# Kernel optimization log

Hardware: AMD Instinct MI355X
Metric: run time of the kernel (lower is better)

Reference implementation:

```python
import jax, jax.numpy as jnp
import numpy as np
import math

# model / graph sizes
N_NODES, N_EDGES = 50000, 400000
IN_DIM, N_HID = 256, 128
NUM_TYPES, NUM_REL = 4, 5
N_HEADS, D_K = 4, 32
N_LAYERS, MAX_LEN = 2, 240
SQRT_DK = math.sqrt(D_K)


def _gelu(x):
    return jax.nn.gelu(x, approximate=False)  # torch F.gelu is exact erf


def _per_type_linear(x, types, W, b):
    # x:[n,din], types:[n] int, W:[T,din,dout], b:[T,dout]
    out = jnp.zeros((x.shape[0], W.shape[-1]), x.dtype)
    for t in range(W.shape[0]):  # small fixed type count
        out = jnp.where((types == t)[:, None], x @ W[t] + b[t], out)
    return out


def setup_inputs() -> dict:
    key = jax.random.key(0)
    ks = jax.random.split(key, 16)
    node_feature = jax.random.normal(ks[0], (N_NODES, IN_DIM), jnp.float32)
    node_type = jax.random.randint(ks[1], (N_NODES,), 0, NUM_TYPES)
    edge_index = jax.random.randint(ks[2], (2, N_EDGES), 0, N_NODES)
    edge_type = jax.random.randint(ks[3], (N_EDGES,), 0, NUM_REL)
    edge_time = jax.random.randint(ks[4], (N_EDGES,), 0, MAX_LEN)

    def w(k, shape, s=0.05):
        return jax.random.normal(k, shape, jnp.float32) * s

    adapt_W = w(ks[5], (NUM_TYPES, IN_DIM, N_HID))
    adapt_b = jnp.zeros((NUM_TYPES, N_HID), jnp.float32)
    Wk = w(ks[6], (N_LAYERS, NUM_TYPES, N_HID, N_HID))
    Wq = w(ks[7], (N_LAYERS, NUM_TYPES, N_HID, N_HID))
    Wv = w(ks[8], (N_LAYERS, NUM_TYPES, N_HID, N_HID))
    Wa = w(ks[9], (N_LAYERS, NUM_TYPES, N_HID, N_HID))
    bk = jnp.zeros((N_LAYERS, NUM_TYPES, N_HID), jnp.float32)
    bq = jnp.zeros((N_LAYERS, NUM_TYPES, N_HID), jnp.float32)
    bv = jnp.zeros((N_LAYERS, NUM_TYPES, N_HID), jnp.float32)
    ba = jnp.zeros((N_LAYERS, NUM_TYPES, N_HID), jnp.float32)
    rel_pri = jnp.ones((N_LAYERS, NUM_REL, N_HEADS), jnp.float32)
    rel_att = w(ks[10], (N_LAYERS, NUM_REL, N_HEADS, D_K, D_K), 0.1) + jnp.eye(D_K, dtype=jnp.float32)
    rel_msg = w(ks[11], (N_LAYERS, NUM_REL, N_HEADS, D_K, D_K), 0.1) + jnp.eye(D_K, dtype=jnp.float32)
    skip = jnp.ones((N_LAYERS, NUM_TYPES), jnp.float32)
    # fixed sinusoidal RTE table (pyHGT RelTemporalEncoding, requires_grad=False)
    pos = np.arange(MAX_LEN, dtype=np.float32)[:, None]
    div = np.exp(np.arange(0, N_HID, 2, dtype=np.float32) * -(math.log(10000.0) / N_HID))
    tab = np.zeros((MAX_LEN, N_HID), np.float32)
    tab[:, 0::2] = np.sin(pos * div) / math.sqrt(N_HID)
    tab[:, 1::2] = np.cos(pos * div) / math.sqrt(N_HID)
    rte_emb = jnp.asarray(tab)
    rte_W = w(ks[12], (N_LAYERS, N_HID, N_HID))
    rte_b = jnp.zeros((N_LAYERS, N_HID), jnp.float32)
    return dict(node_feature=node_feature, adapt_W=adapt_W, adapt_b=adapt_b,
                Wk=Wk, bk=bk, Wq=Wq, bq=bq, Wv=Wv, bv=bv, Wa=Wa, ba=ba,
                rel_pri=rel_pri, rel_att=rel_att, rel_msg=rel_msg, skip=skip,
                rte_emb=rte_emb, rte_W=rte_W, rte_b=rte_b,
                node_type=node_type, edge_index=edge_index,
                edge_type=edge_type, edge_time=edge_time)


def reference(node_feature, adapt_W, adapt_b, Wk, bk, Wq, bq, Wv, bv, Wa, ba,
              rel_pri, rel_att, rel_msg, skip, rte_emb, rte_W, rte_b,
              node_type, edge_index, edge_type, edge_time):
    n = node_feature.shape[0]
    src, dst = edge_index[0], edge_index[1]  # PyG: row0 = source j, row1 = target i
    st, tt = node_type[src], node_type[dst]
    # per-type input adaptation (all types use Linear + GELU)
    h = _gelu(_per_type_linear(node_feature, node_type, adapt_W, adapt_b))  # [N, n_hid]
    for l in range(N_LAYERS):  # HGTConv stack
        x_j, x_i = h[src], h[dst]
        s_e = x_j + rte_emb[edge_time] @ rte_W[l] + rte_b[l]  # RTE on source per edge
        k = _per_type_linear(s_e, st, Wk[l], bk[l]).reshape(-1, N_HEADS, D_K)
        v = _per_type_linear(s_e, st, Wv[l], bv[l]).reshape(-1, N_HEADS, D_K)
        q = _per_type_linear(x_i, tt, Wq[l], bq[l]).reshape(-1, N_HEADS, D_K)
        att = jnp.zeros((k.shape[0], N_HEADS), h.dtype)
        msg = jnp.zeros_like(v)
        for r in range(NUM_REL):  # small fixed relation count
            m = edge_type == r
            kr = jnp.einsum('ehd,hdk->ehk', k, rel_att[l, r])
            ar = jnp.einsum('ehd,ehd->eh', q, kr) * rel_pri[l, r] / SQRT_DK
            mr = jnp.einsum('ehd,hdk->ehk', v, rel_msg[l, r])
            att = jnp.where(m[:, None], ar, att)
            msg = jnp.where(m[:, None, None], mr, msg)
        # segment softmax over incoming edges of each target node
        amax = jax.lax.stop_gradient(jax.ops.segment_max(att, dst, num_segments=n))
        ex = jnp.exp(att - amax[dst])
        denom = jax.ops.segment_sum(ex, dst, num_segments=n)
        alpha = ex / (denom[dst] + 1e-16)
        aggr = jax.ops.segment_sum((msg * alpha[:, :, None]).reshape(-1, N_HEADS * D_K),
                                   dst, num_segments=n)  # [N, n_hid]
        g = _gelu(aggr)
        res = jnp.zeros_like(h)
        for t in range(NUM_TYPES):  # per-type output transform + gated skip
            a_t = jax.nn.sigmoid(skip[l, t])
            res = jnp.where((node_type == t)[:, None],
                            (g @ Wa[l, t] + ba[l, t]) * a_t + h * (1.0 - a_t), res)
        h = res
    return h
```

## Files before the change

### kernel.cpp

```cpp
#include <hip/hip_runtime.h>
#include <math.h>

#define NN     50000
#define NE     400000
#define INDIM  256
#define NH     128
#define NTYPE  4
#define NREL   5
#define NHEAD  4
#define DK     32
#define RSQRT_DK 0.17677669529663687f
#define BN     64
#define NSCAN_BLK ((NN + 255) / 256)
#define XB     260

__device__ __forceinline__ float gelu_f(float x){
    return 0.5f * x * (1.0f + erff(x * 0.70710678118654752f));
}

__global__ void GNN_nscatter(const int* __restrict__ ntype, int* __restrict__ ncur,
                             int* __restrict__ nperm){
    __shared__ int lcnt[4], lbase[4];
    int tid = threadIdx.x;
    if (tid < 4) lcnt[tid] = 0;
    __syncthreads();
    int n = blockIdx.x * 256 + tid;
    int t = 0, lpos = 0;
    bool ok = (n < NN);
    if (ok){ t = ntype[n]; lpos = atomicAdd(&lcnt[t], 1); }
    __syncthreads();
    if (tid < 4 && lcnt[tid] > 0) lbase[tid] = atomicAdd(&ncur[tid], lcnt[tid]);
    __syncthreads();
    if (ok) nperm[t * NN + lbase[t] + lpos] = n;
}

__global__ void GNN_deg(const int* __restrict__ edst, int* __restrict__ deg){
    int e = blockIdx.x * 256 + threadIdx.x;
    if (e < NE) atomicAdd(&deg[edst[e]], 1);
}

__global__ void GNN_scan1(const int* __restrict__ deg, int* __restrict__ rowptr,
                          int* __restrict__ bsum){
    __shared__ int s[256];
    int g = blockIdx.x * 256 + threadIdx.x;
    int v = (g < NN) ? deg[g] : 0;
    s[threadIdx.x] = v;
    __syncthreads();
    for (int off = 1; off < 256; off <<= 1){
        int t = (threadIdx.x >= off) ? s[threadIdx.x - off] : 0;
        __syncthreads();
        s[threadIdx.x] += t;
        __syncthreads();
    }
    if (g < NN) rowptr[g] = s[threadIdx.x] - v;
    if (threadIdx.x == 255) bsum[blockIdx.x] = s[255];
}

__global__ void GNN_scan2(const int* __restrict__ bsum, int* __restrict__ bbase){
    __shared__ int s[256];
    int v = (threadIdx.x < NSCAN_BLK) ? bsum[threadIdx.x] : 0;
    s[threadIdx.x] = v;
    __syncthreads();
    for (int off = 1; off < 256; off <<= 1){
        int t = (threadIdx.x >= off) ? s[threadIdx.x - off] : 0;
        __syncthreads();
        s[threadIdx.x] += t;
        __syncthreads();
    }
    bbase[threadIdx.x] = s[threadIdx.x] - v;
}

__global__ void GNN_scan3(int* __restrict__ rowptr, const int* __restrict__ bbase){
    int g = blockIdx.x * 256 + threadIdx.x;
    if (g < NN) rowptr[g] += bbase[blockIdx.x];
    if (g == 0) rowptr[NN] = NE;
}

__global__ void GNN_csr_scatter(const int* __restrict__ edst, const int* __restrict__ rowptr,
                                int* __restrict__ cursor, int* __restrict__ csr_e){
    int e = blockIdx.x * 256 + threadIdx.x;
    if (e >= NE) return;
    int d = edst[e];
    int pos = atomicAdd(&cursor[d], 1);
    csr_e[rowptr[d] + pos] = e;
}

template<int MODE>
__device__ __forceinline__ void gemm_tile(
    const float* __restrict__ X, int K,
    const float* __restrict__ W, const float* __restrict__ brow,
    float a_t, const float* __restrict__ Hprev,
    float* Xs, float* Ws, const int* nids,
    float* __restrict__ OUT)
{
    int tid = threadIdx.x;
    int cq = tid & 31, rq = tid >> 5;

    int xc0 = tid >> 6,          xr0i = tid & 63;
    int xc1 = (256 + tid) >> 6,  xr1i = tid & 63;
    int nid0 = nids[xr0i], nid1 = nids[xr1i];
    const float* xp0 = (nid0 >= 0) ? X + (size_t)nid0 * K + xc0 * 4 : nullptr;
    const float* xp1 = (nid1 >= 0) ? X + (size_t)nid1 * K + xc1 * 4 : nullptr;
    int wk = tid >> 5, wc4 = (tid & 31) * 4;

    float4 xr0, xr1, wr0, wr1, wr2, wr3;
    const float4 z4 = make_float4(0.f, 0.f, 0.f, 0.f);

    #define LOADREGS(k0)                                                        \
        xr0 = xp0 ? *(const float4*)(xp0 + (k0)) : z4;                          \
        xr1 = xp1 ? *(const float4*)(xp1 + (k0)) : z4;                          \
        wr0 = *(const float4*)(W + (size_t)((k0) + wk     ) * NH + wc4);        \
        wr1 = *(const float4*)(W + (size_t)((k0) + wk +  8) * NH + wc4);        \
        wr2 = *(const float4*)(W + (size_t)((k0) + wk + 16) * NH + wc4);        \
        wr3 = *(const float4*)(W + (size_t)((k0) + wk + 24) * NH + wc4);

    #define WRITELDS()                                                          \
        *(float4*)&Xs[xc0 * XB + xr0i * 4] = xr0;                               \
        *(float4*)&Xs[xc1 * XB + xr1i * 4] = xr1;                               \
        *(float4*)&Ws[(wk     ) * 128 + wc4] = wr0;                             \
        *(float4*)&Ws[(wk +  8) * 128 + wc4] = wr1;                             \
        *(float4*)&Ws[(wk + 16) * 128 + wc4] = wr2;                             \
        *(float4*)&Ws[(wk + 24) * 128 + wc4] = wr3;

    float acc[8][4];
    #pragma unroll
    for (int i = 0; i < 8; i++){ acc[i][0]=0.f; acc[i][1]=0.f; acc[i][2]=0.f; acc[i][3]=0.f; }

    LOADREGS(0);
    for (int k0 = 0; k0 < K; k0 += 32){
        WRITELDS();
        __syncthreads();
        if (k0 + 32 < K){ LOADREGS(k0 + 32); }
        #pragma unroll 2
        for (int c4 = 0; c4 < 8; c4++){
            float4 w0 = *(const float4*)&Ws[(c4*4+0)*128 + cq*4];
            float4 w1 = *(const float4*)&Ws[(c4*4+1)*128 + cq*4];
            float4 w2 = *(const float4*)&Ws[(c4*4+2)*128 + cq*4];
            float4 w3 = *(const float4*)&Ws[(c4*4+3)*128 + cq*4];
            #pragma unroll
            for (int i = 0; i < 8; i++){
                float4 xv = *(const float4*)&Xs[c4 * XB + (rq + 8*i) * 4];
                acc[i][0] += xv.x*w0.x + xv.y*w1.x + xv.z*w2.x + xv.w*w3.x;
                acc[i][1] += xv.x*w0.y + xv.y*w1.y + xv.z*w2.y + xv.w*w3.y;
                acc[i][2] += xv.x*w0.z + xv.y*w1.z + xv.z*w2.z + xv.w*w3.z;
                acc[i][3] += xv.x*w0.w + xv.y*w1.w + xv.z*w2.w + xv.w*w3.w;
            }
        }
        __syncthreads();
    }
    #undef LOADREGS
    #undef WRITELDS

    float4 b4 = *(const float4*)(brow + cq * 4);
    float one_m = 1.f - a_t;
    #pragma unroll
    for (int i = 0; i < 8; i++){
        int r = rq + 8*i;
        int nid = nids[r];
        if (nid < 0) continue;
        float v0 = acc[i][0] + b4.x, v1 = acc[i][1] + b4.y;
        float v2 = acc[i][2] + b4.z, v3 = acc[i][3] + b4.w;
        if (MODE == 0){ v0 = gelu_f(v0); v1 = gelu_f(v1); v2 = gelu_f(v2); v3 = gelu_f(v3); }
        if (MODE == 2){
            float4 hp = *(const float4*)(Hprev + (size_t)nid * NH + cq * 4);
            v0 = v0 * a_t + hp.x * one_m; v1 = v1 * a_t + hp.y * one_m;
            v2 = v2 * a_t + hp.z * one_m; v3 = v3 * a_t + hp.w * one_m;
        }
        *(float4*)(OUT + (size_t)nid * NH + cq * 4) = make_float4(v0, v1, v2, v3);
    }
}

template<int MODE>
__global__ __launch_bounds__(256) void GNN_ptype_gemm(
    const float* __restrict__ X, int K,
    const float* __restrict__ Wall, const float* __restrict__ ball,
    const float* __restrict__ skiprow, const float* __restrict__ Hprev,
    const int* __restrict__ nperm, const int* __restrict__ counts,
    float* __restrict__ OUT)
{
    int t = blockIdx.y;
    int cnt = counts[t];
    int rbase = blockIdx.x * BN;
    if (rbase >= cnt) return;
    __shared__ float Xs[8 * XB];
    __shared__ float Ws[32 * 128];
    __shared__ int nids[BN];
    int tid = threadIdx.x;
    if (tid < BN){
        int idx = rbase + tid;
        nids[tid] = (idx < cnt) ? nperm[t * NN + idx] : -1;
    }
    __syncthreads();
    float a_t = 0.f;
    if (MODE == 2) a_t = 1.f / (1.f + expf(-skiprow[t]));
    gemm_tile<MODE>(X, K, Wall + (size_t)t * K * NH, ball + t * NH,
                    a_t, Hprev, Xs, Ws, nids, OUT);
}

__global__ __launch_bounds__(256) void GNN_qkv_gemm(
    const float* __restrict__ X,
    const float* __restrict__ Wq, const float* __restrict__ bq,
    const float* __restrict__ Wk, const float* __restrict__ bk,
    const float* __restrict__ Wv, const float* __restrict__ bv,
    const int* __restrict__ nperm, const int* __restrict__ counts,
    float* __restrict__ Qn, float* __restrict__ Kn, float* __restrict__ Vn)
{
    int t = blockIdx.y;
    int cnt = counts[t];
    int rbase = blockIdx.x * BN;
    if (rbase >= cnt) return;
    __shared__ float Xs[8 * XB];
    __shared__ float Ws[32 * 128];
    __shared__ int nids[BN];
    int tid = threadIdx.x;
    if (tid < BN){
        int idx = rbase + tid;
        nids[tid] = (idx < cnt) ? nperm[t * NN + idx] : -1;
    }
    __syncthreads();
    int z = blockIdx.z;
    const float* W = (z == 0) ? Wq : (z == 1) ? Wk : Wv;
    const float* b = (z == 0) ? bq : (z == 1) ? bk : bv;
    float* OUT     = (z == 0) ? Qn : (z == 1) ? Kn : Vn;
    gemm_tile<1>(X, NH, W + (size_t)t * NH * NH, b + t * NH,
                 0.f, nullptr, Xs, Ws, nids, OUT);
}

__global__ void GNN_rte_tab(const float* __restrict__ rte_emb, const float* __restrict__ rW,
                            const float* __restrict__ rb, float* __restrict__ tab){
    int m = blockIdx.x, j = threadIdx.x;
    __shared__ float e[NH];
    e[j] = rte_emb[m * NH + j];
    __syncthreads();
    float a = rb[j];
    #pragma unroll 8
    for (int d = 0; d < NH; d++) a += e[d] * rW[d * NH + j];
    tab[m * NH + j] = a;
}

__global__ void GNN_rte_proj(const float* __restrict__ tab, const float* __restrict__ WkL,
                             const float* __restrict__ WvL, float* __restrict__ RK,
                             float* __restrict__ RV){
    int m = blockIdx.x, j = threadIdx.x;
    int sel = blockIdx.y; int t = sel >> 1; int which = sel & 1;
    const float* W = (which ? WvL : WkL) + (size_t)t * NH * NH;
    float* O = which ? RV : RK;
    __shared__ float e[NH];
    e[j] = tab[m * NH + j];
    __syncthreads();
    float a = 0.f;
    #pragma unroll 8
    for (int d = 0; d < NH; d++) a += e[d] * W[d * NH + j];
    O[(size_t)(t * 240 + m) * NH + j] = a;
}

__global__ __launch_bounds__(256) void GNN_qa(
    const float* __restrict__ Qn, const float* __restrict__ relA, float* __restrict__ QA)
{
    __shared__ float Atp[4 * 1072];
    int r = blockIdx.y;
    int nb = blockIdx.x * 64;
    int tid = threadIdx.x;
    const float* Ar = relA + (size_t)r * NHEAD * DK * DK;
    for (int x = tid; x < NHEAD * DK * DK; x += 256){
        int hh = x >> 10, rem = x & 1023, dd = rem >> 5, cc = rem & 31;
        Atp[hh * 1072 + (dd >> 2) * 132 + cc * 4 + (dd & 3)] = Ar[x];
    }
    __syncthreads();
    int cq = tid & 31, rq = tid >> 5;
    int h = cq >> 3;
    int abase = h * 1072 + (cq & 7) * 132;
    int rowoff[8];
    #pragma unroll
    for (int i = 0; i < 8; i++){
        int node = nb + rq + 8*i;
        if (node >= NN) node = NN - 1;
        rowoff[i] = node * NH + h * 32;
    }
    float acc[8][4];
    #pragma unroll
    for (int i = 0; i < 8; i++){ acc[i][0]=0.f; acc[i][1]=0.f; acc[i][2]=0.f; acc[i][3]=0.f; }
    #pragma unroll 2
    for (int c4 = 0; c4 < 8; c4++){
        float4 av0 = *(const float4*)&Atp[abase + c4 * 16 + 0];
        float4 av1 = *(const float4*)&Atp[abase + c4 * 16 + 4];
        float4 av2 = *(const float4*)&Atp[abase + c4 * 16 + 8];
        float4 av3 = *(const float4*)&Atp[abase + c4 * 16 + 12];
        #pragma unroll
        for (int i = 0; i < 8; i++){
            float4 qv = *(const float4*)(Qn + rowoff[i] + c4 * 4);
            acc[i][0] += qv.x*av0.x + qv.y*av1.x + qv.z*av2.x + qv.w*av3.x;
            acc[i][1] += qv.x*av0.y + qv.y*av1.y + qv.z*av2.y + qv.w*av3.y;
            acc[i][2] += qv.x*av0.z + qv.y*av1.z + qv.z*av2.z + qv.w*av3.z;
            acc[i][3] += qv.x*av0.w + qv.y*av1.w + qv.z*av2.w + qv.w*av3.w;
        }
    }
    #pragma unroll
    for (int i = 0; i < 8; i++){
        int node = nb + rq + 8*i;
        if (node >= NN) continue;
        *(float4*)(QA + ((size_t)r * NN + node) * NH + cq * 4) =
            make_float4(acc[i][0], acc[i][1], acc[i][2], acc[i][3]);
    }
}

__global__ __launch_bounds__(256) void GNN_edge_att(
    const float* __restrict__ Kn, const float* __restrict__ RK, const float* __restrict__ QA,
    const int* __restrict__ esrc, const int* __restrict__ edst,
    const int* __restrict__ etype, const int* __restrict__ etime,
    const int* __restrict__ ntype, const float* __restrict__ relP,
    float* __restrict__ att)
{
    int tid = threadIdx.x;
    int e = blockIdx.x * 8 + (tid >> 5);
    if (e >= NE) return;
    int lane = tid & 31;
    int s = esrc[e], d = edst[e], r = etype[e], tm = etime[e];
    int st = ntype[s];
    float4 k4 = *(const float4*)(Kn + (size_t)s * NH + lane * 4);
    float4 rk = *(const float4*)(RK + (size_t)(st * 240 + tm) * NH + lane * 4);
    float4 qa = *(const float4*)(QA + ((size_t)r * NN + d) * NH + lane * 4);
    float pv = (k4.x + rk.x) * qa.x + (k4.y + rk.y) * qa.y
             + (k4.z + rk.z) * qa.z + (k4.w + rk.w) * qa.w;
    pv += __shfl_xor(pv, 4);
    pv += __shfl_xor(pv, 2);
    pv += __shfl_xor(pv, 1);
    if ((lane & 7) == 0){
        int head = lane >> 3;
        att[(size_t)e * NHEAD + head] = pv * relP[r * NHEAD + head] * RSQRT_DK;
    }
}

__global__ __launch_bounds__(256) void GNN_node_aggr(
    const float* __restrict__ att, const float* __restrict__ Vn, const float* __restrict__ RV,
    const int* __restrict__ rowptr, const int* __restrict__ csr_e,
    const int* __restrict__ esrc, const int* __restrict__ etype,
    const int* __restrict__ etime, const int* __restrict__ ntype,
    float* __restrict__ P)
{
    int tid = threadIdx.x;
    int i = blockIdx.x * 8 + (tid >> 5);
    if (i >= NN) return;
    int lane = tid & 31;
    int head = lane >> 3;
    int beg = rowptr[i], end = rowptr[i + 1];
    float mx = -3.4e38f;
    for (int k = beg; k < end; k++){
        int e = csr_e[k];
        mx = fmaxf(mx, att[(size_t)e * NHEAD + head]);
    }
    float4 acc[NREL];
    #pragma unroll
    for (int rr = 0; rr < NREL; rr++) acc[rr] = make_float4(0.f, 0.f, 0.f, 0.f);
    float den = 0.f;
    for (int k = beg; k < end; k++){
        int e = csr_e[k];
        int s = esrc[e], r = etype[e], tm = etime[e];
        int st = ntype[s];
        float ex = expf(att[(size_t)e * NHEAD + head] - mx);
        den += ex;
        float4 v4 = *(const float4*)(Vn + (size_t)s * NH + lane * 4);
        float4 rv = *(const float4*)(RV + (size_t)(st * 240 + tm) * NH + lane * 4);
        float vx = v4.x + rv.x, vy = v4.y + rv.y, vz = v4.z + rv.z, vw = v4.w + rv.w;
        #pragma unroll
        for (int rr = 0; rr < NREL; rr++){
            float w = (rr == r) ? ex : 0.f;
            acc[rr].x += w * vx; acc[rr].y += w * vy;
            acc[rr].z += w * vz; acc[rr].w += w * vw;
        }
    }
    float inv = 1.f / (den + 1e-16f);
    #pragma unroll
    for (int rr = 0; rr < NREL; rr++){
        *(float4*)(P + ((size_t)rr * NN + i) * NH + lane * 4) =
            make_float4(acc[rr].x * inv, acc[rr].y * inv, acc[rr].z * inv, acc[rr].w * inv);
    }
}

__global__ __launch_bounds__(256) void GNN_pm(
    const float* __restrict__ P, const float* __restrict__ relM, float* __restrict__ aggr)
{
    __shared__ float Msp[2][4 * 1072];
    int tid = threadIdx.x;
    int nb = blockIdx.x * 64;
    int cq = tid & 31, rq = tid >> 5;
    int h = cq >> 3;
    int mbase = h * 1072 + (cq & 7) * 132;
    int rowoff[8];
    #pragma unroll
    for (int i = 0; i < 8; i++){
        int node = nb + rq + 8*i;
        if (node >= NN) node = NN - 1;
        rowoff[i] = node * NH + h * 32;
    }
    float acc[8][4];
    #pragma unroll
    for (int i = 0; i < 8; i++){ acc[i][0]=0.f; acc[i][1]=0.f; acc[i][2]=0.f; acc[i][3]=0.f; }

    #pragma unroll
    for (int j = 0; j < 4; j++){
        int s = tid + 256 * j;
        float4 mv = *(const float4*)(relM + 4 * s);
        *(float4*)&Msp[0][(s >> 8) * 1072 + (s & 7) * 132 + ((s >> 3) & 31) * 4] = mv;
    }
    __syncthreads();

    #pragma unroll
    for (int r = 0; r < NREL; r++){
        float4 mpre[4];
        if (r + 1 < NREL){
            const float* Mn = relM + (size_t)(r + 1) * NHEAD * DK * DK;
            #pragma unroll
            for (int j = 0; j < 4; j++)
                mpre[j] = *(const float4*)(Mn + 4 * (tid + 256 * j));
        }
        const float* Ms = Msp[r & 1];
        const float* Pr = P + (size_t)r * NN * NH;
        #pragma unroll 2
        for (int d4 = 0; d4 < 8; d4++){
            float4 mv0 = *(const float4*)&Ms[mbase + d4 * 16 + 0];
            float4 mv1 = *(const float4*)&Ms[mbase + d4 * 16 + 4];
            float4 mv2 = *(const float4*)&Ms[mbase + d4 * 16 + 8];
            float4 mv3 = *(const float4*)&Ms[mbase + d4 * 16 + 12];
            #pragma unroll
            for (int i = 0; i < 8; i++){
                float4 pv = *(const float4*)(Pr + rowoff[i] + d4 * 4);
                acc[i][0] += pv.x*mv0.x + pv.y*mv1.x + pv.z*mv2.x + pv.w*mv3.x;
                acc[i][1] += pv.x*mv0.y + pv.y*mv1.y + pv.z*mv2.y + pv.w*mv3.y;
                acc[i][2] += pv.x*mv0.z + pv.y*mv1.z + pv.z*mv2.z + pv.w*mv3.z;
                acc[i][3] += pv.x*mv0.w + pv.y*mv1.w + pv.z*mv2.w + pv.w*mv3.w;
            }
        }
        if (r + 1 < NREL){
            #pragma unroll
            for (int j = 0; j < 4; j++){
                int s = tid + 256 * j;
                *(float4*)&Msp[(r + 1) & 1][(s >> 8) * 1072 + (s & 7) * 132 +
                                            ((s >> 3) & 31) * 4] = mpre[j];
            }
            __syncthreads();
        }
    }
    #pragma unroll
    for (int i = 0; i < 8; i++){
        int node = nb + rq + 8*i;
        if (node >= NN) continue;
        *(float4*)(aggr + (size_t)node * NH + cq * 4) =
            make_float4(gelu_f(acc[i][0]), gelu_f(acc[i][1]),
                        gelu_f(acc[i][2]), gelu_f(acc[i][3]));
    }
}

extern "C" void kernel_launch(void* const* d_in, const int* in_sizes, int n_in,
                              void* d_out, int out_size, void* d_ws, size_t ws_size,
                              hipStream_t stream)
{
    const float* node_feature = (const float*)d_in[0];
    const float* adapt_W = (const float*)d_in[1];
    const float* adapt_b = (const float*)d_in[2];
    const float* Wk = (const float*)d_in[3];
    const float* bk = (const float*)d_in[4];
    const float* Wq = (const float*)d_in[5];
    const float* bq = (const float*)d_in[6];
    const float* Wv = (const float*)d_in[7];
    const float* bv = (const float*)d_in[8];
    const float* Wa = (const float*)d_in[9];
    const float* ba = (const float*)d_in[10];
    const float* rel_pri = (const float*)d_in[11];
    const float* rel_att = (const float*)d_in[12];
    const float* rel_msg = (const float*)d_in[13];
    const float* skip = (const float*)d_in[14];
    const float* rte_emb = (const float*)d_in[15];
    const float* rte_W = (const float*)d_in[16];
    const float* rte_b = (const float*)d_in[17];
    const int* node_type = (const int*)d_in[18];
    const int* edge_index = (const int*)d_in[19];
    const int* edge_type = (const int*)d_in[20];
    const int* edge_time = (const int*)d_in[21];
    const int* esrc = edge_index;
    const int* edst = edge_index + NE;

    char* p = (char*)d_ws;
    auto alloc = [&](size_t bytes) -> char* {
        char* r = p; p += (bytes + 255) & ~(size_t)255; return r;
    };
    float* hA    = (float*)alloc((size_t)NN * NH * 4);
    float* Qn    = (float*)alloc((size_t)NN * NH * 4);
    float* Kn    = (float*)alloc((size_t)NN * NH * 4);
    float* Vn    = (float*)alloc((size_t)NN * NH * 4);
    float* QA    = (float*)alloc((size_t)NREL * NN * NH * 4);
    float* rtab  = (float*)alloc((size_t)240 * NH * 4);
    float* RK    = (float*)alloc((size_t)NTYPE * 240 * NH * 4);
    float* RV    = (float*)alloc((size_t)NTYPE * 240 * NH * 4);
    int* nperm   = (int*)alloc((size_t)NTYPE * NN * 4);
    int* rowptr  = (int*)alloc((size_t)(NN + 1) * 4);
    int* csr_e   = (int*)alloc((size_t)NE * 4);
    int* deg     = (int*)alloc((size_t)2 * NN * 4);
    int* cursor  = deg + NN;
    int* bsum    = (int*)alloc(256 * 4);
    int* bbase   = (int*)alloc(256 * 4);
    int* ncur    = (int*)alloc(64);
    float* att   = Qn;
    float* Pbuf  = QA;
    float* aggr  = Kn;

    hipMemsetAsync(ncur, 0, 64, stream);
    hipMemsetAsync(deg, 0, (size_t)2 * NN * 4, stream);

    GNN_nscatter<<<(NN + 255) / 256, 256, 0, stream>>>(node_type, ncur, nperm);
    GNN_deg<<<(NE + 255) / 256, 256, 0, stream>>>(edst, deg);
    GNN_scan1<<<NSCAN_BLK, 256, 0, stream>>>(deg, rowptr, bsum);
    GNN_scan2<<<1, 256, 0, stream>>>(bsum, bbase);
    GNN_scan3<<<NSCAN_BLK, 256, 0, stream>>>(rowptr, bbase);
    GNN_csr_scatter<<<(NE + 255) / 256, 256, 0, stream>>>(edst, rowptr, cursor, csr_e);

    dim3 ggrid((NN + BN - 1) / BN, NTYPE);
    GNN_ptype_gemm<0><<<ggrid, 256, 0, stream>>>(node_feature, INDIM, adapt_W, adapt_b,
                                                 nullptr, nullptr, nperm, ncur, hA);
    const float* hin = hA;
    for (int l = 0; l < 2; l++){
        const float* WkL = Wk + (size_t)l * NTYPE * NH * NH;
        const float* WqL = Wq + (size_t)l * NTYPE * NH * NH;
        const float* WvL = Wv + (size_t)l * NTYPE * NH * NH;
        const float* WaL = Wa + (size_t)l * NTYPE * NH * NH;
        const float* bkL = bk + (size_t)l * NTYPE * NH;
        const float* bqL = bq + (size_t)l * NTYPE * NH;
        const float* bvL = bv + (size_t)l * NTYPE * NH;
        const float* baL = ba + (size_t)l * NTYPE * NH;
        const float* relA = rel_att + (size_t)l * NREL * NHEAD * DK * DK;
        const float* relM = rel_msg + (size_t)l * NREL * NHEAD * DK * DK;
        const float* relP = rel_pri + (size_t)l * NREL * NHEAD;

        GNN_rte_tab<<<240, 128, 0, stream>>>(rte_emb, rte_W + (size_t)l * NH * NH,
                                             rte_b + (size_t)l * NH, rtab);
        GNN_rte_proj<<<dim3(240, NTYPE * 2), 128, 0, stream>>>(rtab, WkL, WvL, RK, RV);

        GNN_qkv_gemm<<<dim3(ggrid.x, NTYPE, 3), 256, 0, stream>>>(
            hin, WqL, bqL, WkL, bkL, WvL, bvL, nperm, ncur, Qn, Kn, Vn);

        GNN_qa<<<dim3((NN + 63) / 64, NREL), 256, 0, stream>>>(Qn, relA, QA);

        GNN_edge_att<<<(NE + 7) / 8, 256, 0, stream>>>(
            Kn, RK, QA, esrc, edst, edge_type, edge_time, node_type, relP, att);

        GNN_node_aggr<<<(NN + 7) / 8, 256, 0, stream>>>(
            att, Vn, RV, rowptr, csr_e, esrc, edge_type, edge_time, node_type, Pbuf);

        GNN_pm<<<(NN + 63) / 64, 256, 0, stream>>>(Pbuf, relM, aggr);

        float* hout = (l == 0) ? hA : (float*)d_out;
        GNN_ptype_gemm<2><<<ggrid, 256, 0, stream>>>(
            aggr, NH, WaL, baL, skip + (size_t)l * NTYPE, hin,
            nperm, ncur, hout);
        hin = hout;
    }
}
```

Baseline: 1.097 ms.

## Double-buffer per-type GEMM tiles via direct global-to-LDS async loads

The per-type GEMM kernel now uses a new tile routine that stages X rows and W tiles straight into shared memory with the global_load_lds builtin. Two buffers are used so the next K-chunk loads while the current one is computed. This aims to hide global memory latency and skip the register round trip of the old staged copy. It doubles LDS use per block, which may reduce occupancy, and it relies on the per-lane 16-byte DMA layout being right.

```diff
diff --git a/kernel.cpp b/kernel.cpp
--- a/kernel.cpp
+++ b/kernel.cpp
@@ -16,6 +16,12 @@
 
 __device__ __forceinline__ float gelu_f(float x){
     return 0.5f * x * (1.0f + erff(x * 0.70710678118654752f));
+}
+
+__device__ __forceinline__ void gload16(const float* g, float* s){
+    __builtin_amdgcn_global_load_lds(
+        (const __attribute__((address_space(1))) void*)g,
+        (__attribute__((address_space(3))) void*)s, 16, 0, 0);
 }
 
 __global__ void GNN_nscatter(const int* __restrict__ ntype, int* __restrict__ ncur,
@@ -171,6 +177,84 @@
 }
 
 template<int MODE>
+__device__ __forceinline__ void gemm_tile_dma(
+    const float* __restrict__ X, int K,
+    const float* __restrict__ W, const float* __restrict__ brow,
+    float a_t, const float* __restrict__ Hprev,
+    float* Xs, float* Ws, const int* nids,
+    float* __restrict__ OUT)
+{
+    int tid = threadIdx.x;
+    int cq = tid & 31, rq = tid >> 5;
+    int lane = tid & 63, w = tid >> 6;
+
+    int nidl = nids[lane]; if (nidl < 0) nidl = 0;
+    const float* xrow  = X + (size_t)nidl * K;
+    const float* wbase = W + lane * 4;
+
+    float acc[8][4];
+    #pragma unroll
+    for (int i = 0; i < 8; i++){ acc[i][0]=0.f; acc[i][1]=0.f; acc[i][2]=0.f; acc[i][3]=0.f; }
+
+    #define STAGE(k0, Xb, Wb)                                                   \
+        gload16(xrow + (k0) + w * 4,       (Xb) + w * 256);                     \
+        gload16(xrow + (k0) + (w + 4) * 4, (Xb) + (w + 4) * 256);               \
+        gload16(wbase + (size_t)((k0) + 2 * (w     )) * NH, (Wb) + (w     ) * 256); \
+        gload16(wbase + (size_t)((k0) + 2 * (w +  4)) * NH, (Wb) + (w +  4) * 256); \
+        gload16(wbase + (size_t)((k0) + 2 * (w +  8)) * NH, (Wb) + (w +  8) * 256); \
+        gload16(wbase + (size_t)((k0) + 2 * (w + 12)) * NH, (Wb) + (w + 12) * 256);
+
+    STAGE(0, Xs, Ws);
+    int buf = 0;
+    for (int k0 = 0; k0 < K; k0 += 32){
+        __syncthreads();
+        if (k0 + 32 < K){
+            float* Xn = Xs + (buf ^ 1) * 2048;
+            float* Wn = Ws + (buf ^ 1) * 4096;
+            STAGE(k0 + 32, Xn, Wn);
+        }
+        const float* Xsb = Xs + buf * 2048;
+        const float* Wsb = Ws + buf * 4096;
+        #pragma unroll 2
+        for (int c4 = 0; c4 < 8; c4++){
+            float4 w0 = *(const float4*)&Wsb[(c4*4+0)*128 + cq*4];
+            float4 w1 = *(const float4*)&Wsb[(c4*4+1)*128 + cq*4];
+            float4 w2 = *(const float4*)&Wsb[(c4*4+2)*128 + cq*4];
+            float4 w3 = *(const float4*)&Wsb[(c4*4+3)*128 + cq*4];
+            #pragma unroll
+            for (int i = 0; i < 8; i++){
+                float4 xv = *(const float4*)&Xsb[c4 * 256 + (rq + 8*i) * 4];
+                acc[i][0] += xv.x*w0.x + xv.y*w1.x + xv.z*w2.x + xv.w*w3.x;
+                acc[i][1] += xv.x*w0.y + xv.y*w1.y + xv.z*w2.y + xv.w*w3.y;
+                acc[i][2] += xv.x*w0.z + xv.y*w1.z + xv.z*w2.z + xv.w*w3.z;
+                acc[i][3] += xv.x*w0.w + xv.y*w1.w + xv.z*w2.w + xv.w*w3.w;
+            }
+        }
+        __syncthreads();
+        buf ^= 1;
+    }
+    #undef STAGE
+
+    float4 b4 = *(const float4*)(brow + cq * 4);
+    float one_m = 1.f - a_t;
+    #pragma unroll
+    for (int i = 0; i < 8; i++){
+        int r = rq + 8*i;
+        int nid = nids[r];
+        if (nid < 0) continue;
+        float v0 = acc[i][0] + b4.x, v1 = acc[i][1] + b4.y;
+        float v2 = acc[i][2] + b4.z, v3 = acc[i][3] + b4.w;
+        if (MODE == 0){ v0 = gelu_f(v0); v1 = gelu_f(v1); v2 = gelu_f(v2); v3 = gelu_f(v3); }
+        if (MODE == 2){
+            float4 hp = *(const float4*)(Hprev + (size_t)nid * NH + cq * 4);
+            v0 = v0 * a_t + hp.x * one_m; v1 = v1 * a_t + hp.y * one_m;
+            v2 = v2 * a_t + hp.z * one_m; v3 = v3 * a_t + hp.w * one_m;
+        }
+        *(float4*)(OUT + (size_t)nid * NH + cq * 4) = make_float4(v0, v1, v2, v3);
+    }
+}
+
+template<int MODE>
 __global__ __launch_bounds__(256) void GNN_ptype_gemm(
     const float* __restrict__ X, int K,
     const float* __restrict__ Wall, const float* __restrict__ ball,
@@ -182,8 +266,8 @@
     int cnt = counts[t];
     int rbase = blockIdx.x * BN;
     if (rbase >= cnt) return;
-    __shared__ float Xs[8 * XB];
-    __shared__ float Ws[32 * 128];
+    __shared__ float Xs[2 * 2048];
+    __shared__ float Ws[2 * 4096];
     __shared__ int nids[BN];
     int tid = threadIdx.x;
     if (tid < BN){
@@ -193,8 +277,8 @@
     __syncthreads();
     float a_t = 0.f;
     if (MODE == 2) a_t = 1.f / (1.f + expf(-skiprow[t]));
-    gemm_tile<MODE>(X, K, Wall + (size_t)t * K * NH, ball + t * NH,
-                    a_t, Hprev, Xs, Ws, nids, OUT);
+    gemm_tile_dma<MODE>(X, K, Wall + (size_t)t * K * NH, ball + t * NH,
+                        a_t, Hprev, Xs, Ws, nids, OUT);
 }
 
 __global__ __launch_bounds__(256) void GNN_qkv_gemm(
```

Result: slower. 1.160 ms (+5.7%).
